# Kernel optimization log

Hardware: AMD Instinct MI355X
Metric: run time of the kernel (lower is better)

Reference implementation:

```python
import jax, jax.numpy as jnp
import numpy as np

N, K, M, H, F = 4, 1024, 1024, 16, 4096
D = M // H  # per-head dim (dim_q = dim_v = 64)
EPS = 1e-5


def _mha(q_in, k_in, v_in, Wq, bq, Wk, bk, Wv, bv, Wo, bo, mask):
    # Wq/Wk/Wv: [H, M, D]; bq/bk/bv: [H, D]; Wo: [H*D, M]; bo: [M]
    q = jnp.einsum('nkm,hmd->nhkd', q_in, Wq) + bq[None, :, None, :]
    k = jnp.einsum('nkm,hmd->nhkd', k_in, Wk) + bk[None, :, None, :]
    v = jnp.einsum('nkm,hmd->nhkd', v_in, Wv) + bv[None, :, None, :]
    scores = jnp.einsum('nhkd,nhld->nhkl', q, k) / jnp.sqrt(jnp.asarray(D, q.dtype))
    if mask is not None:
        scores = jnp.where(mask[:, None, :, :] == 0, jnp.asarray(-jnp.inf, q.dtype), scores)
    attn = jax.nn.softmax(scores, axis=-1)          # [N,H,K,K]
    y = jnp.einsum('nhkl,nhld->nhkd', attn, v)      # [N,H,K,D]
    y = y.transpose(0, 2, 1, 3).reshape(q_in.shape[0], q_in.shape[1], -1)  # concat heads -> [N,K,H*D]
    return y @ Wo + bo


def _ln(x, g, b):
    mu = jnp.mean(x, axis=-1, keepdims=True)
    var = jnp.mean((x - mu) ** 2, axis=-1, keepdims=True)
    return (x - mu) * jax.lax.rsqrt(var + EPS) * g + b


def setup_inputs() -> dict:
    key = jax.random.key(0)
    ks = jax.random.split(key, 24)
    s = 0.02
    def rn(k, shape):
        return jax.random.normal(k, shape, dtype=jnp.float32) * s
    inp = {
        'dec_inp': jax.random.normal(ks[0], (N, K, M), dtype=jnp.float32),
        'enc_out': jax.random.normal(ks[1], (N, K, M), dtype=jnp.float32),
        'mask': jnp.tril(jnp.ones((K, K), dtype=jnp.int32))[None].repeat(N, axis=0),
        # self-attention params
        'Wq_s': rn(ks[2], (H, M, D)), 'bq_s': jnp.zeros((H, D)),
        'Wk_s': rn(ks[3], (H, M, D)), 'bk_s': jnp.zeros((H, D)),
        'Wv_s': rn(ks[4], (H, M, D)), 'bv_s': jnp.zeros((H, D)),
        'Wo_s': rn(ks[5], (H * D, M)), 'bo_s': jnp.zeros((M,)),
        # cross-attention params
        'Wq_c': rn(ks[6], (H, M, D)), 'bq_c': jnp.zeros((H, D)),
        'Wk_c': rn(ks[7], (H, M, D)), 'bk_c': jnp.zeros((H, D)),
        'Wv_c': rn(ks[8], (H, M, D)), 'bv_c': jnp.zeros((H, D)),
        'Wo_c': rn(ks[9], (H * D, M)), 'bo_c': jnp.zeros((M,)),
        # feedforward params
        'W1': rn(ks[10], (M, F)), 'b1': jnp.zeros((F,)),
        'W2': rn(ks[11], (F, M)), 'b2': jnp.zeros((M,)),
        # layernorm params
        'g1': jnp.ones((M,)), 'be1': jnp.zeros((M,)),
        'g2': jnp.ones((M,)), 'be2': jnp.zeros((M,)),
        'g3': jnp.ones((M,)), 'be3': jnp.zeros((M,)),
    }
    return inp


def reference(dec_inp, enc_out, mask,
              Wq_s, bq_s, Wk_s, bk_s, Wv_s, bv_s, Wo_s, bo_s,
              Wq_c, bq_c, Wk_c, bk_c, Wv_c, bv_c, Wo_c, bo_c,
              W1, b1, W2, b2, g1, be1, g2, be2, g3, be3):
    # masked self-attention + residual + LN (dropout = identity in eval)
    out1 = _mha(dec_inp, dec_inp, dec_inp, Wq_s, bq_s, Wk_s, bk_s, Wv_s, bv_s, Wo_s, bo_s, mask)
    out2 = _ln(dec_inp + out1, g1, be1)
    # cross-attention with encoder output + residual + LN
    out3 = _mha(out2, enc_out, enc_out, Wq_c, bq_c, Wk_c, bk_c, Wv_c, bv_c, Wo_c, bo_c, None)
    out4 = _ln(out3 + out2, g2, be2)
    # feedforward + residual + LN
    out5 = jax.nn.relu(out4 @ W1 + b1) @ W2 + b2
    return _ln(out5 + out4, g3, be3)
```

## Files before the change

### kernel.cpp

```cpp
#include <hip/hip_runtime.h>

#define NB   4
#define SEQ  1024
#define MD   1024
#define NH   16
#define HD   64
#define FF   4096
#define NK   (NB*SEQ)
#define EPSF 1e-5f
#define QS   3072

typedef short short8 __attribute__((ext_vector_type(8)));
typedef float f32x4  __attribute__((ext_vector_type(4)));
typedef unsigned short u16;
typedef unsigned int u32;

__device__ __forceinline__ u16 f2bf(float x) {
    union { float f; unsigned u; } v; v.f = x;
    unsigned r = v.u + 0x7FFF + ((v.u >> 16) & 1);
    return (u16)(r >> 16);
}
__device__ __forceinline__ u16 f2bf_trunc(float x) {
    union { float f; unsigned u; } v; v.f = x;
    return (u16)(v.u >> 16);
}
__device__ __forceinline__ float bf2f(u16 x) {
    union { unsigned u; float f; } v; v.u = ((unsigned)x) << 16;
    return v.f;
}
__device__ __forceinline__ void gload_lds16(const void* g, void* l) {
    __builtin_amdgcn_global_load_lds(
        (const __attribute__((address_space(1))) unsigned int*)g,
        (__attribute__((address_space(3))) unsigned int*)l,
        16, 0, 0);
}

__global__ __launch_bounds__(256) void conv_bf16(const float* __restrict__ s0,
                                                 const float* __restrict__ s1,
                                                 u16* __restrict__ d0,
                                                 u16* __restrict__ d1) {
    const float* S = blockIdx.y ? s1 : s0;
    u16* D = blockIdx.y ? d1 : d0;
    const int i = blockIdx.x * 256 + threadIdx.x;
    float4 v = ((const float4*)S)[i];
    ushort4 o;
    o.x = f2bf(v.x); o.y = f2bf(v.y); o.z = f2bf(v.z); o.w = f2bf(v.w);
    ((ushort4*)D)[i] = o;
}

__global__ __launch_bounds__(256) void mask_tiles(const int* __restrict__ mask,
                                                  int* __restrict__ cls,
                                                  u32* __restrict__ bits) {
    const int jt = blockIdx.x, qt = blockIdx.y, n = blockIdx.z;
    const int t = threadIdx.x;
    const int r = t >> 1, h2 = (t & 1) * 2;
    u32 bb[2];
#pragma unroll
    for (int sg = 0; sg < 2; ++sg) {
        const int* mp = &mask[((size_t)n * SEQ + qt * 128 + r) * SEQ + jt * 128 + (h2 + sg) * 32];
        u32 b = 0;
#pragma unroll
        for (int k = 0; k < 8; ++k) {
            int4 v = *(const int4*)(mp + k * 4);
            b |= (v.x ? 1u : 0u) << (k * 4 + 0);
            b |= (v.y ? 1u : 0u) << (k * 4 + 1);
            b |= (v.z ? 1u : 0u) << (k * 4 + 2);
            b |= (v.w ? 1u : 0u) << (k * 4 + 3);
        }
        bb[sg] = b;
    }
    const int tile = (n * 8 + qt) * 8 + jt;
    bits[((size_t)tile * 128 + r) * 4 + h2]     = bb[0];
    bits[((size_t)tile * 128 + r) * 4 + h2 + 1] = bb[1];
    const int nfull  = __syncthreads_count(bb[0] == 0xFFFFFFFFu && bb[1] == 0xFFFFFFFFu);
    const int nempty = __syncthreads_count(bb[0] == 0u && bb[1] == 0u);
    if (t == 0) cls[tile] = (nfull == 256) ? 2 : ((nempty == 256) ? 0 : 1);
}

struct QkvArgs { const float* src[6]; u16* dst[6]; };

__global__ __launch_bounds__(256) void repack_qkv(QkvArgs a) {
    const int m0 = blockIdx.x * 64;
    const int h  = blockIdx.y;
    const int w  = blockIdx.z;
    const float* W = a.src[w];
    u16* BT = a.dst[w];
    const int t = threadIdx.x;
    __shared__ u16 Ts[64][72];

    const int r = t >> 4, c4 = (t & 15) * 4;
#pragma unroll
    for (int p = 0; p < 4; ++p) {
        const int row = r + p * 16;
        float4 v = *(const float4*)&W[((size_t)h * 1024 + m0 + row) * 64 + c4];
        Ts[row][c4] = f2bf(v.x); Ts[row][c4 + 1] = f2bf(v.y);
        Ts[row][c4 + 2] = f2bf(v.z); Ts[row][c4 + 3] = f2bf(v.w);
    }
    __syncthreads();
    const int d = t >> 2, j0 = (t & 3) * 16;
#pragma unroll
    for (int p = 0; p < 4; ++p) {
        ushort4 o;
        o.x = Ts[j0 + p * 4 + 0][d]; o.y = Ts[j0 + p * 4 + 1][d];
        o.z = Ts[j0 + p * 4 + 2][d]; o.w = Ts[j0 + p * 4 + 3][d];
        *(ushort4*)&BT[((size_t)h * 64 + d) * 1024 + m0 + j0 + p * 4] = o;
    }
}

struct FD { const float* src; int ss; u16* dst; int ds; };
struct FlatArgs { FD d[10]; };

__global__ __launch_bounds__(256) void repack_flat(FlatArgs fa) {
    FD u = fa.d[blockIdx.z];
    const int r0 = blockIdx.x * 64;
    const int c0 = blockIdx.y * 64;
    const int t  = threadIdx.x;
    __shared__ u16 Ts[64][72];

    const int r = t >> 4, c4 = (t & 15) * 4;
#pragma unroll
    for (int p = 0; p < 4; ++p) {
        const int row = r + p * 16;
        float4 v = *(const float4*)&u.src[(size_t)(r0 + row) * u.ss + c0 + c4];
        Ts[row][c4] = f2bf(v.x); Ts[row][c4 + 1] = f2bf(v.y);
        Ts[row][c4 + 2] = f2bf(v.z); Ts[row][c4 + 3] = f2bf(v.w);
    }
    __syncthreads();
    const int d = t >> 2, j0 = (t & 3) * 16;
#pragma unroll
    for (int p = 0; p < 4; ++p) {
        ushort4 o;
        o.x = Ts[j0 + p * 4 + 0][d]; o.y = Ts[j0 + p * 4 + 1][d];
        o.z = Ts[j0 + p * 4 + 2][d]; o.w = Ts[j0 + p * 4 + 3][d];
        *(ushort4*)&u.dst[(size_t)(c0 + d) * u.ds + r0 + j0 + p * 4] = o;
    }
}

template<int OUT_BF16, int RELU, int RESID, int BIAS3, int PARTIAL, int VT>
__global__ __launch_bounds__(256) void gemm_mfma(const u16* __restrict__ A,
                                                 const u16* __restrict__ A2,
                                                 int Astride,
                                                 const u16* __restrict__ BT,
                                                 int Bstride,
                                                 const float* __restrict__ b0,
                                                 const float* __restrict__ b1p,
                                                 const float* __restrict__ b2p,
                                                 const float* __restrict__ resid,
                                                 void* __restrict__ Cout,
                                                 u16* __restrict__ VtOut,
                                                 int Kd, int Nd) {
    const int nt = blockIdx.x;
    const int mt = blockIdx.y;
    const int t  = threadIdx.x;
    const int wave = t >> 6, lane = t & 63;
    const int q = lane >> 4, l16 = lane & 15;
    const int wm = wave >> 1, wn = wave & 1;

    __shared__ __align__(16) u16 As[128 * 64];
    __shared__ __align__(16) u16 Bs[128 * 64];

    const int row0 = mt * 128, col0 = nt * 128;
    const u16* Ause = (col0 < 1024) ? A : A2;
    const int kBase = PARTIAL ? blockIdx.z * Kd : 0;

    f32x4 acc[4][4];
#pragma unroll
    for (int r = 0; r < 4; ++r)
#pragma unroll
        for (int c = 0; c < 4; ++c) acc[r][c] = (f32x4)0.0f;

    const int lrow = lane >> 3;
    const int lcb  = lane & 7;

    for (int k0 = 0; k0 < Kd; k0 += 64) {
        __syncthreads();
#pragma unroll
        for (int p = 0; p < 4; ++p) {
            const int rr = wave * 32 + p * 8 + lrow;
            const int gcb = lcb ^ (rr & 7);
            gload_lds16(Ause + (size_t)(row0 + rr) * Astride + kBase + k0 + gcb * 8, As + (size_t)(wave * 32 + p * 8) * 64);
            gload_lds16(BT   + (size_t)(col0 + rr) * Bstride + kBase + k0 + gcb * 8, Bs + (size_t)(wave * 32 + p * 8) * 64);
        }
        __syncthreads();

#pragma unroll
        for (int s = 0; s < 2; ++s) {
            const int pb = (q + s * 4) ^ (l16 & 7);
            short8 af[4], bf[4];
#pragma unroll
            for (int r = 0; r < 4; ++r)
                af[r] = *(const short8*)&As[(wm * 64 + r * 16 + l16) * 64 + pb * 8];
#pragma unroll
            for (int c = 0; c < 4; ++c)
                bf[c] = *(const short8*)&Bs[(wn * 64 + c * 16 + l16) * 64 + pb * 8];
#pragma unroll
            for (int r = 0; r < 4; ++r)
#pragma unroll
                for (int c = 0; c < 4; ++c)
                    acc[r][c] = __builtin_amdgcn_mfma_f32_16x16x32_bf16(af[r], bf[c], acc[r][c], 0, 0, 0);
        }
    }

    float* Pout = PARTIAL ? ((float*)Cout + (size_t)blockIdx.z * NK * Nd) : nullptr;

#pragma unroll
    for (int c = 0; c < 4; ++c) {
        const int col = col0 + wn * 64 + c * 16 + l16;
        float bb = 0.0f;
        if (!PARTIAL) {
            if (BIAS3) {
                const int sec = col >> 10;
                const float* bp = sec == 0 ? b0 : (sec == 1 ? b1p : b2p);
                bb = bp[col & 1023];
            } else {
                bb = b0[col];
            }
        }
#pragma unroll
        for (int r = 0; r < 4; ++r) {
#pragma unroll
            for (int reg = 0; reg < 4; ++reg) {
                const int row = row0 + wm * 64 + r * 16 + q * 4 + reg;
                float v = acc[r][c][reg] + bb;
                if (PARTIAL) {
                    Pout[(size_t)row * Nd + col] = acc[r][c][reg];
                } else {
                    if (RELU)  v = fmaxf(v, 0.0f);
                    if (RESID) v += resid[(size_t)row * Nd + col];
                    if (OUT_BF16) ((u16*)Cout)[(size_t)row * Nd + col] = f2bf(v);
                    else          ((float*)Cout)[(size_t)row * Nd + col] = v;
                }
            }
        }
    }
}

template<int OUT_BF16, int RELU, int BIAS3, int PARTIAL, int VT>
__global__ __launch_bounds__(512, 2) void gemm256p(const u16* __restrict__ A,
                                                   const u16* __restrict__ A2,
                                                   int Astride,
                                                   const u16* __restrict__ BT,
                                                   int Bstride,
                                                   const float* __restrict__ b0,
                                                   const float* __restrict__ b1p,
                                                   const float* __restrict__ b2p,
                                                   void* __restrict__ Cout,
                                                   u16* __restrict__ VtOut,
                                                   int Kd, int Nd, int swzW) {
    const int t  = threadIdx.x;
    const int wave = t >> 6, lane = t & 63;
    const int q = lane >> 4, l16 = lane & 15;
    const int wm = wave >> 1, wn = wave & 1;
    const int x7 = l16 & 7;

    const int gx = gridDim.x;
    const int bid = blockIdx.x + blockIdx.y * gx;
    const int cpx = (gx * gridDim.y) >> 3;
    const int xcd = bid & 7;
    const int cc  = bid >> 3;
    const int regNX = gx / swzW;
    const int mtspan = cpx / swzW;
    const int nt = (xcd % regNX) * swzW + cc % swzW;
    const int mt = (xcd / regNX) * mtspan + cc / swzW;

    extern __shared__ __align__(16) char smem[];
    u16* As = (u16*)smem;
    u16* Bs = (u16*)(smem + 3 * 256 * 64 * 2);

    const int row0 = mt * 256, col0 = nt * 128;
    const u16* Ause = (col0 < 1024) ? A : A2;
    const int kBase = PARTIAL ? blockIdx.z * Kd : 0;

    f32x4 acc[4][4];
#pragma unroll
    for (int r = 0; r < 4; ++r)
#pragma unroll
        for (int c = 0; c < 4; ++c) acc[r][c] = (f32x4)0.0f;

    const int lrow = lane >> 3;
    const int lcb  = lane & 7;

    auto stagePart = [&](int slot, int kk, int part) {
#pragma unroll
        for (int p = 0; p < 2; ++p) {
            const int rr = wave * 32 + (part * 2 + p) * 8 + lrow;
            const int gcb = lcb ^ (rr & 7);
            gload_lds16(Ause + (size_t)(row0 + rr) * Astride + kk + gcb * 8,
                        As + slot * (256 * 64) + (wave * 32 + (part * 2 + p) * 8) * 64);
        }
        {
            const int rr = wave * 16 + part * 8 + lrow;
            const int gcb = lcb ^ (rr & 7);
            gload_lds16(BT + (size_t)(col0 + rr) * Bstride + kk + gcb * 8,
                        Bs + slot * (128 * 64) + (wave * 16 + part * 8) * 64);
        }
    };

    const int nsteps = Kd / 64;
    stagePart(0, kBase, 0);      stagePart(0, kBase, 1);
    stagePart(1, kBase + 64, 0); stagePart(1, kBase + 64, 1);

    int st = 0, st2 = 2;
    for (int it = 0; it < nsteps; ++it) {
        if (it + 1 < nsteps) asm volatile("s_waitcnt vmcnt(6)" ::: "memory");
        else                 asm volatile("s_waitcnt vmcnt(0)" ::: "memory");
        __builtin_amdgcn_s_barrier();

        const u16* Ab = As + st * (256 * 64);
        const u16* Bb = Bs + st * (128 * 64);
        const int pb0 = q ^ x7;
        const int pb1 = (q + 4) ^ x7;

        short8 af0[4], bf0[4], af1[4], bf1[4];
#pragma unroll
        for (int r = 0; r < 4; ++r) {
            af0[r] = *(const short8*)&Ab[(wm * 64 + r * 16 + l16) * 64 + pb0 * 8];
            af1[r] = *(const short8*)&Ab[(wm * 64 + r * 16 + l16) * 64 + pb1 * 8];
        }
#pragma unroll
        for (int c = 0; c < 4; ++c) {
            bf0[c] = *(const short8*)&Bb[(wn * 64 + c * 16 + l16) * 64 + pb0 * 8];
            bf1[c] = *(const short8*)&Bb[(wn * 64 + c * 16 + l16) * 64 + pb1 * 8];
        }

        const bool pre = (it + 2 < nsteps);
        const int kk2 = kBase + (it + 2) * 64;
        if (pre) stagePart(st2, kk2, 0);

        __builtin_amdgcn_s_setprio(1);
#pragma unroll
        for (int r = 0; r < 4; ++r)
#pragma unroll
            for (int c = 0; c < 4; ++c)
                acc[r][c] = __builtin_amdgcn_mfma_f32_16x16x32_bf16(af0[r], bf0[c], acc[r][c], 0, 0, 0);
        __builtin_amdgcn_s_setprio(0);

        if (pre) stagePart(st2, kk2, 1);

        __builtin_amdgcn_s_setprio(1);
#pragma unroll
        for (int r = 0; r < 4; ++r)
#pragma unroll
            for (int c = 0; c < 4; ++c)
                acc[r][c] = __builtin_amdgcn_mfma_f32_16x16x32_bf16(af1[r], bf1[c], acc[r][c], 0, 0, 0);
        __builtin_amdgcn_s_setprio(0);

        st  = (st  == 2) ? 0 : st + 1;
        st2 = (st2 == 2) ? 0 : st2 + 1;
    }

    if (VT && col0 >= 2048) {
#pragma unroll
        for (int c = 0; c < 4; ++c) {
            const int col = col0 + wn * 64 + c * 16 + l16;
            const float bb = b2p[col & 1023];
            const int d = col & 63, hh = (col >> 6) & 15;
#pragma unroll
            for (int r = 0; r < 4; ++r) {
                const int row = row0 + wm * 64 + r * 16 + q * 4;
                const int nn = row >> 10, k = row & 1023;
                ushort4 o;
                o.x = f2bf(acc[r][c][0] + bb);
                o.y = f2bf(acc[r][c][1] + bb);
                o.z = f2bf(acc[r][c][2] + bb);
                o.w = f2bf(acc[r][c][3] + bb);
                *(ushort4*)&VtOut[((size_t)(nn * 16 + hh) * 64 + d) * 1024 + k] = o;
            }
        }
        return;
    }

    float* Pout = PARTIAL ? ((float*)Cout + (size_t)blockIdx.z * NK * Nd) : nullptr;

#pragma unroll
    for (int c = 0; c < 4; ++c) {
        const int col = col0 + wn * 64 + c * 16 + l16;
        float bb = 0.0f;
        if (!PARTIAL) {
            if (BIAS3) {
                const int sec = col >> 10;
                const float* bp = sec == 0 ? b0 : (sec == 1 ? b1p : b2p);
                bb = bp[col & 1023];
            } else {
                bb = b0[col];
            }
        }
#pragma unroll
        for (int r = 0; r < 4; ++r) {
#pragma unroll
            for (int reg = 0; reg < 4; ++reg) {
                const int row = row0 + wm * 64 + r * 16 + q * 4 + reg;
                float v = acc[r][c][reg] + bb;
                if (PARTIAL) {
                    Pout[(size_t)row * Nd + col] = acc[r][c][reg];
                } else {
                    if (RELU)  v = fmaxf(v, 0.0f);
                    if (OUT_BF16) ((u16*)Cout)[(size_t)row * Nd + col] = f2bf(v);
                    else          ((float*)Cout)[(size_t)row * Nd + col] = v;
                }
            }
        }
    }
}

#define PSTR 136
#define ATTN_LDS (128*64*2 + 64*128*2 + 8*16*PSTR*2)

__global__ __launch_bounds__(512, 4) void attn_mfma(const u16* __restrict__ QKV,
                                                    const u16* __restrict__ Vt,
                                                    const int* __restrict__ cls,
                                                    const u32* __restrict__ bits,
                                                    u16* __restrict__ Yout) {
    const int h  = blockIdx.x;
    const int n  = blockIdx.z;
    const int qt = (n & 2) ? 7 - (int)blockIdx.y : (int)blockIdx.y;
    const int t  = threadIdx.x;
    const int wave = t >> 6;
    const int lane = t & 63;
    const int quad = lane >> 4;
    const int l16  = lane & 15;
    const int sw   = wave >> 2;
    const int wq   = wave & 3;

    extern __shared__ __align__(16) char smem[];
    u16* Ks = (u16*)smem;
    u16* Vs = (u16*)(smem + 128 * 64 * 2);
    u16* Pw = (u16*)(smem + 128 * 64 * 2 + 64 * 128 * 2) + wave * 16 * PSTR;

    const int bh = n * NH + h;
    const int i0 = qt * 128;

    int cl[8];
    if (cls) {
        const int* cp = &cls[(n * 8 + qt) * 8];
#pragma unroll
        for (int j = 0; j < 8; ++j) cl[j] = cp[j];
    } else {
#pragma unroll
        for (int j = 0; j < 8; ++j) cl[j] = 2;
    }

    short8 qf[2];
    {
        const u16* qrow = QKV + ((size_t)n * SEQ + i0 + sw * 64 + wq * 16 + l16) * QS + h * 64 + quad * 8;
        short8 a = *(const short8*)(qrow);
        short8 b = *(const short8*)(qrow + 32);
#pragma unroll
        for (int j = 0; j < 8; ++j) {
            qf[0][j] = (short)f2bf(bf2f((u16)a[j]) * 0.18033688f);
            qf[1][j] = (short)f2bf(bf2f((u16)b[j]) * 0.18033688f);
        }
    }

    f32x4 O[4];
#pragma unroll
    for (int d = 0; d < 4; ++d) O[d] = (f32x4)0.0f;
    float lrow[4] = {};

    const int krow = lane >> 3, kblk = lane & 7;
    const int vrow = lane >> 4, vblk = lane & 15;
    const int x7 = l16 & 7;

    for (int jt = 0; jt < SEQ / 128; ++jt) {
        const int c = cl[jt];
        if (c == 0) continue;
        __syncthreads();

#pragma unroll
        for (int p = 0; p < 2; ++p) {
            const int rr = wave * 16 + p * 8 + krow;
            const int kb = kblk ^ (rr & 7);
            gload_lds16(QKV + ((size_t)n * SEQ + jt * 128 + rr) * QS + 1024 + h * 64 + kb * 8,
                        Ks + (wave * 16 + p * 8) * 64);
        }
#pragma unroll
        for (int p = 0; p < 2; ++p) {
            const int rr = wave * 8 + p * 4 + vrow;
            const int kb = vblk ^ (rr & 15);
            gload_lds16(Vt + ((size_t)bh * HD + rr) * SEQ + jt * 128 + kb * 8,
                        Vs + (wave * 8 + p * 4) * 128);
        }
        __syncthreads();

        f32x4 S[8];
#pragma unroll
        for (int sub = 0; sub < 8; ++sub) {
            S[sub] = (f32x4)0.0f;
            const int row = sub * 16 + l16;
            short8 k0 = *(const short8*)&Ks[row * 64 + ((quad ^ x7) * 8)];
            S[sub] = __builtin_amdgcn_mfma_f32_16x16x32_bf16(qf[0], k0, S[sub], 0, 0, 0);
            short8 k1 = *(const short8*)&Ks[row * 64 + (((4 + quad) ^ x7) * 8)];
            S[sub] = __builtin_amdgcn_mfma_f32_16x16x32_bf16(qf[1], k1, S[sub], 0, 0, 0);
        }

        if (c == 1) {
#pragma unroll
            for (int reg = 0; reg < 4; ++reg) {
                const int row = sw * 64 + wq * 16 + quad * 4 + reg;
                const uint4 mm = *(const uint4*)&bits[((size_t)((n * 8 + qt) * 8 + jt) * 128 + row) * 4];
#pragma unroll
                for (int sub = 0; sub < 8; ++sub) {
                    const u32 seg = (sub >> 1) == 0 ? mm.x : (sub >> 1) == 1 ? mm.y : (sub >> 1) == 2 ? mm.z : mm.w;
                    if (!((seg >> ((sub & 1) * 16 + l16)) & 1u)) S[sub][reg] = -1e30f;
                }
            }
        }

#pragma unroll
        for (int reg = 0; reg < 4; ++reg) {
            float rs = 0.0f;
#pragma unroll
            for (int sub = 0; sub < 8; ++sub) {
                float e = exp2f(S[sub][reg]);
                Pw[(quad * 4 + reg) * PSTR + sub * 16 + l16] = f2bf_trunc(e);
                rs += e;
            }
            rs += __shfl_xor(rs, 1);
            rs += __shfl_xor(rs, 2);
            rs += __shfl_xor(rs, 4);
            rs += __shfl_xor(rs, 8);
            lrow[reg] += rs;
        }

        short8 pa[4];
#pragma unroll
        for (int ks = 0; ks < 4; ++ks)
            pa[ks] = *(const short8*)&Pw[l16 * PSTR + ks * 32 + quad * 8];
#pragma unroll
        for (int d = 0; d < 4; ++d) {
            const int row = d * 16 + l16;
#pragma unroll
            for (int ks = 0; ks < 4; ++ks) {
                short8 vb = *(const short8*)&Vs[row * 128 + (((ks * 4 + quad) ^ l16) & 15) * 8];
                O[d] = __builtin_amdgcn_mfma_f32_16x16x32_bf16(pa[ks], vb, O[d], 0, 0, 0);
            }
        }
    }

#pragma unroll
    for (int d = 0; d < 4; ++d) {
#pragma unroll
        for (int reg = 0; reg < 4; ++reg) {
            const int row = i0 + sw * 64 + wq * 16 + quad * 4 + reg;
            const int col = h * 64 + d * 16 + l16;
            Yout[((size_t)n * SEQ + row) * QS + col] = f2bf(O[d][reg] / lrow[reg]);
        }
    }
}

__global__ __launch_bounds__(256) void ln_kernel(const float* __restrict__ X,
                                                 const float* __restrict__ g,
                                                 const float* __restrict__ be,
                                                 float* __restrict__ Y,
                                                 u16* __restrict__ Yb) {
    const int row = blockIdx.x;
    const int t = threadIdx.x;
    __shared__ float red[256];

    const float4 v = ((const float4*)(X + (size_t)row * MD))[t];
    red[t] = v.x + v.y + v.z + v.w;
    __syncthreads();
    for (int s2 = 128; s2 > 0; s2 >>= 1) {
        if (t < s2) red[t] += red[t + s2];
        __syncthreads();
    }
    const float mu = red[0] * (1.0f / MD);
    __syncthreads();

    float dx = v.x - mu, dy = v.y - mu, dz = v.z - mu, dw = v.w - mu;
    red[t] = dx * dx + dy * dy + dz * dz + dw * dw;
    __syncthreads();
    for (int s2 = 128; s2 > 0; s2 >>= 1) {
        if (t < s2) red[t] += red[t + s2];
        __syncthreads();
    }
    const float var = red[0] * (1.0f / MD);
    const float rs = rsqrtf(var + EPSF);

    const float4 gv = ((const float4*)g)[t];
    const float4 bv = ((const float4*)be)[t];
    float4 o;
    o.x = dx * rs * gv.x + bv.x;
    o.y = dy * rs * gv.y + bv.y;
    o.z = dz * rs * gv.z + bv.z;
    o.w = dw * rs * gv.w + bv.w;
    if (Y) ((float4*)(Y + (size_t)row * MD))[t] = o;
    if (Yb) {
        ushort4 ob;
        ob.x = f2bf(o.x); ob.y = f2bf(o.y); ob.z = f2bf(o.z); ob.w = f2bf(o.w);
        ((ushort4*)(Yb + (size_t)row * MD))[t] = ob;
    }
}

__global__ __launch_bounds__(256) void ln_fused2(const float* __restrict__ p0,
                                                 const float* __restrict__ p1,
                                                 const float* __restrict__ bias,
                                                 const float* __restrict__ resid,
                                                 const float* __restrict__ g,
                                                 const float* __restrict__ be,
                                                 float* __restrict__ Y) {
    const int row = blockIdx.x;
    const int t = threadIdx.x;
    __shared__ float red[256];

    const float4 a = ((const float4*)(p0 + (size_t)row * MD))[t];
    const float4 b = ((const float4*)(p1 + (size_t)row * MD))[t];
    const float4 r = ((const float4*)(resid + (size_t)row * MD))[t];
    const float4 bi = ((const float4*)bias)[t];
    float4 v;
    v.x = a.x + b.x + r.x + bi.x;
    v.y = a.y + b.y + r.y + bi.y;
    v.z = a.z + b.z + r.z + bi.z;
    v.w = a.w + b.w + r.w + bi.w;

    red[t] = v.x + v.y + v.z + v.w;
    __syncthreads();
    for (int s2 = 128; s2 > 0; s2 >>= 1) {
        if (t < s2) red[t] += red[t + s2];
        __syncthreads();
    }
    const float mu = red[0] * (1.0f / MD);
    __syncthreads();

    float dx = v.x - mu, dy = v.y - mu, dz = v.z - mu, dw = v.w - mu;
    red[t] = dx * dx + dy * dy + dz * dz + dw * dw;
    __syncthreads();
    for (int s2 = 128; s2 > 0; s2 >>= 1) {
        if (t < s2) red[t] += red[t + s2];
        __syncthreads();
    }
    const float var = red[0] * (1.0f / MD);
    const float rs = rsqrtf(var + EPSF);

    const float4 gv = ((const float4*)g)[t];
    const float4 bv = ((const float4*)be)[t];
    float4 o;
    o.x = dx * rs * gv.x + bv.x;
    o.y = dy * rs * gv.y + bv.y;
    o.z = dz * rs * gv.z + bv.z;
    o.w = dw * rs * gv.w + bv.w;
    ((float4*)(Y + (size_t)row * MD))[t] = o;
}

extern "C" void kernel_launch(void* const* d_in, const int* in_sizes, int n_in,
                              void* d_out, int out_size, void* d_ws, size_t ws_size,
                              hipStream_t stream) {
    const float* dec  = (const float*)d_in[0];
    const float* enc  = (const float*)d_in[1];
    const int*   mask = (const int*)d_in[2];
    const float* Wq_s = (const float*)d_in[3];
    const float* bq_s = (const float*)d_in[4];
    const float* Wk_s = (const float*)d_in[5];
    const float* bk_s = (const float*)d_in[6];
    const float* Wv_s = (const float*)d_in[7];
    const float* bv_s = (const float*)d_in[8];
    const float* Wo_s = (const float*)d_in[9];
    const float* bo_s = (const float*)d_in[10];
    const float* Wq_c = (const float*)d_in[11];
    const float* bq_c = (const float*)d_in[12];
    const float* Wk_c = (const float*)d_in[13];
    const float* bk_c = (const float*)d_in[14];
    const float* Wv_c = (const float*)d_in[15];
    const float* bv_c = (const float*)d_in[16];
    const float* Wo_c = (const float*)d_in[17];
    const float* bo_c = (const float*)d_in[18];
    const float* W1   = (const float*)d_in[19];
    const float* b1   = (const float*)d_in[20];
    const float* W2   = (const float*)d_in[21];
    const float* b2   = (const float*)d_in[22];
    const float* g1   = (const float*)d_in[23];
    const float* be1  = (const float*)d_in[24];
    const float* g2   = (const float*)d_in[25];
    const float* be2  = (const float*)d_in[26];
    const float* g3   = (const float*)d_in[27];
    const float* be3  = (const float*)d_in[28];

    char* wsb = (char*)d_ws;
    const size_t MB = 1u << 20;
    u16*   decb  = (u16*)(wsb + 0 * MB);
    u16*   O2b   = (u16*)(wsb + 0 * MB);
    u16*   encb  = (u16*)(wsb + 8 * MB);
    u16*   O4b   = (u16*)(wsb + 8 * MB);
    u16*   WqkvsT= (u16*)(wsb + 16 * MB);
    u16*   WqkvcT= (u16*)(wsb + 22 * MB);
    u16*   WosT  = (u16*)(wsb + 28 * MB);
    u16*   WocT  = (u16*)(wsb + 30 * MB);
    u16*   W1T   = (u16*)(wsb + 32 * MB);
    u16*   W2T   = (u16*)(wsb + 40 * MB);
    u16*   QKVb  = (u16*)(wsb + 48 * MB);
    u16*   Vt    = (u16*)(wsb + 72 * MB);
    u16*   Hb    = (u16*)(wsb + 48 * MB);
    int*   mcls  = (int*)(wsb + 80 * MB);
    u32*   mbits = (u32*)(wsb + 80 * MB + 64 * 1024);
    float* Tb    = (float*)(wsb + 80 * MB);
    float* FP    = (float*)(wsb + 0 * MB);
    float* O2    = (float*)(wsb + 96 * MB);
    float* O4    = (float*)(wsb + 96 * MB);

    dim3 blk(256);
    dim3 blkA(512);
    dim3 blkG(512);
    dim3 gConv(NK * MD / 4 / 256, 2);
    dim3 gMask(8, 8, 4);
    dim3 gQkvW(16, 16, 6);
    dim3 gFlatW(16, 16, 10);
    dim3 gAttn(NH, SEQ / 128, NB);
    dim3 gQKV(QS / 128, NK / 256);
    dim3 gOut(MD / 128, NK / 128);
    dim3 gF1(FF / 128, NK / 256);
    dim3 gF2(MD / 128, NK / 256, 2);
    const int GP_LDS = 3 * (256 * 64 + 128 * 64) * 2;

    conv_bf16<<<gConv, blk, 0, stream>>>(dec, enc, decb, encb);
    mask_tiles<<<gMask, blk, 0, stream>>>(mask, mcls, mbits);

    QkvArgs qa;
    qa.src[0] = Wq_s; qa.src[1] = Wk_s; qa.src[2] = Wv_s;
    qa.src[3] = Wq_c; qa.src[4] = Wk_c; qa.src[5] = Wv_c;
    qa.dst[0] = WqkvsT;                 qa.dst[1] = WqkvsT + (size_t)1024 * 1024;
    qa.dst[2] = WqkvsT + (size_t)2048 * 1024;
    qa.dst[3] = WqkvcT;                 qa.dst[4] = WqkvcT + (size_t)1024 * 1024;
    qa.dst[5] = WqkvcT + (size_t)2048 * 1024;
    repack_qkv<<<gQkvW, blk, 0, stream>>>(qa);

    FlatArgs fa;
    fa.d[0] = { Wo_s, 1024, WosT, 1024 };
    fa.d[1] = { Wo_c, 1024, WocT, 1024 };
    for (int u = 0; u < 4; ++u)
        fa.d[2 + u] = { W1 + (size_t)u * 1024, 4096, W1T + (size_t)u * 1024 * 1024, 1024 };
    for (int u = 0; u < 4; ++u)
        fa.d[6 + u] = { W2 + (size_t)u * 1024 * 1024, 1024, W2T + (size_t)u * 1024, 4096 };
    repack_flat<<<gFlatW, blk, 0, stream>>>(fa);

    gemm256p<1, 0, 1, 0, 1><<<gQKV, blkG, GP_LDS, stream>>>(decb, decb, MD, WqkvsT, MD, bq_s, bk_s, bv_s, QKVb, Vt, MD, QS, 6);
    attn_mfma<<<gAttn, blkA, ATTN_LDS, stream>>>(QKVb, Vt, mcls, mbits, QKVb);
    gemm_mfma<0, 0, 1, 0, 0, 0><<<gOut, blk, 0, stream>>>(QKVb, QKVb, QS, WosT, MD, bo_s, nullptr, nullptr, dec, Tb, nullptr, MD, MD);
    ln_kernel<<<NK, blk, 0, stream>>>(Tb, g1, be1, O2, O2b);

    gemm256p<1, 0, 1, 0, 1><<<gQKV, blkG, GP_LDS, stream>>>(O2b, encb, MD, WqkvcT, MD, bq_c, bk_c, bv_c, QKVb, Vt, MD, QS, 6);
    attn_mfma<<<gAttn, blkA, ATTN_LDS, stream>>>(QKVb, Vt, nullptr, nullptr, QKVb);
    gemm_mfma<0, 0, 1, 0, 0, 0><<<gOut, blk, 0, stream>>>(QKVb, QKVb, QS, WocT, MD, bo_c, nullptr, nullptr, O2, Tb, nullptr, MD, MD);
    ln_kernel<<<NK, blk, 0, stream>>>(Tb, g2, be2, O4, O4b);

    gemm256p<1, 1, 0, 0, 0><<<gF1, blkG, GP_LDS, stream>>>(O4b, O4b, MD, W1T, MD, b1, nullptr, nullptr, Hb, nullptr, MD, FF, 8);
    gemm256p<0, 0, 0, 1, 0><<<gF2, blkG, GP_LDS, stream>>>(Hb, Hb, FF, W2T, FF, nullptr, nullptr, nullptr, FP, nullptr, FF / 2, MD, 2);
    ln_fused2<<<NK, blk, 0, stream>>>(FP, FP + (size_t)NK * MD, b2, O4, g3, be3, (float*)d_out);
}
```

Baseline: 325.0 us.

## Route output projections through pipelined GEMM and double-buffer attention K/V tiles

The output-projection GEMMs switch from the simple 128x128 kernel to the triple-buffered 256x128 kernel, which gains a residual-add template flag so the older kernel can be removed. The attention kernel now processes 64-wide key tiles with double-buffered async loads of K and V, prefetching the next tile while computing the current one. This targets load latency stalls in both kernels. The cost is more barriers per key tile in attention and fewer blocks in the output GEMMs (128 instead of 256), which may underfill the GPU.

```diff
diff --git a/kernel.cpp b/kernel.cpp
--- a/kernel.cpp
+++ b/kernel.cpp
@@ -136,30 +136,40 @@
     }
 }
 
-template<int OUT_BF16, int RELU, int RESID, int BIAS3, int PARTIAL, int VT>
-__global__ __launch_bounds__(256) void gemm_mfma(const u16* __restrict__ A,
-                                                 const u16* __restrict__ A2,
-                                                 int Astride,
-                                                 const u16* __restrict__ BT,
-                                                 int Bstride,
-                                                 const float* __restrict__ b0,
-                                                 const float* __restrict__ b1p,
-                                                 const float* __restrict__ b2p,
-                                                 const float* __restrict__ resid,
-                                                 void* __restrict__ Cout,
-                                                 u16* __restrict__ VtOut,
-                                                 int Kd, int Nd) {
-    const int nt = blockIdx.x;
-    const int mt = blockIdx.y;
+template<int OUT_BF16, int RELU, int BIAS3, int PARTIAL, int VT, int RESID>
+__global__ __launch_bounds__(512, 2) void gemm256p(const u16* __restrict__ A,
+                                                   const u16* __restrict__ A2,
+                                                   int Astride,
+                                                   const u16* __restrict__ BT,
+                                                   int Bstride,
+                                                   const float* __restrict__ b0,
+                                                   const float* __restrict__ b1p,
+                                                   const float* __restrict__ b2p,
+                                                   const float* __restrict__ resid,
+                                                   void* __restrict__ Cout,
+                                                   u16* __restrict__ VtOut,
+                                                   int Kd, int Nd, int swzW) {
     const int t  = threadIdx.x;
     const int wave = t >> 6, lane = t & 63;
     const int q = lane >> 4, l16 = lane & 15;
     const int wm = wave >> 1, wn = wave & 1;
-
-    __shared__ __align__(16) u16 As[128 * 64];
-    __shared__ __align__(16) u16 Bs[128 * 64];
-
-    const int row0 = mt * 128, col0 = nt * 128;
+    const int x7 = l16 & 7;
+
+    const int gx = gridDim.x;
+    const int bid = blockIdx.x + blockIdx.y * gx;
+    const int cpx = (gx * gridDim.y) >> 3;
+    const int xcd = bid & 7;
+    const int cc  = bid >> 3;
+    const int regNX = gx / swzW;
+    const int mtspan = cpx / swzW;
+    const int nt = (xcd % regNX) * swzW + cc % swzW;
+    const int mt = (xcd / regNX) * mtspan + cc / swzW;
+
+    extern __shared__ __align__(16) char smem[];
+    u16* As = (u16*)smem;
+    u16* Bs = (u16*)(smem + 3 * 256 * 64 * 2);
+
+    const int row0 = mt * 256, col0 = nt * 128;
     const u16* Ause = (col0 < 1024) ? A : A2;
     const int kBase = PARTIAL ? blockIdx.z * Kd : 0;
 
@@ -172,33 +182,94 @@
     const int lrow = lane >> 3;
     const int lcb  = lane & 7;
 
-    for (int k0 = 0; k0 < Kd; k0 += 64) {
-        __syncthreads();
-#pragma unroll
-        for (int p = 0; p < 4; ++p) {
-            const int rr = wave * 32 + p * 8 + lrow;
+    auto stagePart = [&](int slot, int kk, int part) {
+#pragma unroll
+        for (int p = 0; p < 2; ++p) {
+            const int rr = wave * 32 + (part * 2 + p) * 8 + lrow;
             const int gcb = lcb ^ (rr & 7);
-            gload_lds16(Ause + (size_t)(row0 + rr) * Astride + kBase + k0 + gcb * 8, As + (size_t)(wave * 32 + p * 8) * 64);
-            gload_lds16(BT   + (size_t)(col0 + rr) * Bstride + kBase + k0 + gcb * 8, Bs + (size_t)(wave * 32 + p * 8) * 64);
-        }
-        __syncthreads();
-
-#pragma unroll
-        for (int s = 0; s < 2; ++s) {
-            const int pb = (q + s * 4) ^ (l16 & 7);
-            short8 af[4], bf[4];
-#pragma unroll
-            for (int r = 0; r < 4; ++r)
-                af[r] = *(const short8*)&As[(wm * 64 + r * 16 + l16) * 64 + pb * 8];
+            gload_lds16(Ause + (size_t)(row0 + rr) * Astride + kk + gcb * 8,
+                        As + slot * (256 * 64) + (wave * 32 + (part * 2 + p) * 8) * 64);
+        }
+        {
+            const int rr = wave * 16 + part * 8 + lrow;
+            const int gcb = lcb ^ (rr & 7);
+            gload_lds16(BT + (size_t)(col0 + rr) * Bstride + kk + gcb * 8,
+                        Bs + slot * (128 * 64) + (wave * 16 + part * 8) * 64);
+        }
+    };
+
+    const int nsteps = Kd / 64;
+    stagePart(0, kBase, 0);      stagePart(0, kBase, 1);
+    stagePart(1, kBase + 64, 0); stagePart(1, kBase + 64, 1);
+
+    int st = 0, st2 = 2;
+    for (int it = 0; it < nsteps; ++it) {
+        if (it + 1 < nsteps) asm volatile("s_waitcnt vmcnt(6)" ::: "memory");
+        else                 asm volatile("s_waitcnt vmcnt(0)" ::: "memory");
+        __builtin_amdgcn_s_barrier();
+
+        const u16* Ab = As + st * (256 * 64);
+        const u16* Bb = Bs + st * (128 * 64);
+        const int pb0 = q ^ x7;
+        const int pb1 = (q + 4) ^ x7;
+
+        short8 af0[4], bf0[4], af1[4], bf1[4];
+#pragma unroll
+        for (int r = 0; r < 4; ++r) {
+            af0[r] = *(const short8*)&Ab[(wm * 64 + r * 16 + l16) * 64 + pb0 * 8];
+            af1[r] = *(const short8*)&Ab[(wm * 64 + r * 16 + l16) * 64 + pb1 * 8];
+        }
+#pragma unroll
+        for (int c = 0; c < 4; ++c) {
+            bf0[c] = *(const short8*)&Bb[(wn * 64 + c * 16 + l16) * 64 + pb0 * 8];
+            bf1[c] = *(const short8*)&Bb[(wn * 64 + c * 16 + l16) * 64 + pb1 * 8];
+        }
+
+        const bool pre = (it + 2 < nsteps);
+        const int kk2 = kBase + (it + 2) * 64;
+        if (pre) stagePart(st2, kk2, 0);
+
+        __builtin_amdgcn_s_setprio(1);
+#pragma unroll
+        for (int r = 0; r < 4; ++r)
 #pragma unroll
             for (int c = 0; c < 4; ++c)
-                bf[c] = *(const short8*)&Bs[(wn * 64 + c * 16 + l16) * 64 + pb * 8];
-#pragma unroll
-            for (int r = 0; r < 4; ++r)
-#pragma unroll
-                for (int c = 0; c < 4; ++c)
-                    acc[r][c] = __builtin_amdgcn_mfma_f32_16x16x32_bf16(af[r], bf[c], acc[r][c], 0, 0, 0);
-        }
+                acc[r][c] = __builtin_amdgcn_mfma_f32_16x16x32_bf16(af0[r], bf0[c], acc[r][c], 0, 0, 0);
+        __builtin_amdgcn_s_setprio(0);
+
+        if (pre) stagePart(st2, kk2, 1);
+
+        __builtin_amdgcn_s_setprio(1);
+#pragma unroll
+        for (int r = 0; r < 4; ++r)
+#pragma unroll
+            for (int c = 0; c < 4; ++c)
+                acc[r][c] = __builtin_amdgcn_mfma_f32_16x16x32_bf16(af1[r], bf1[c], acc[r][c], 0, 0, 0);
+        __builtin_amdgcn_s_setprio(0);
+
+        st  = (st  == 2) ? 0 : st + 1;
+        st2 = (st2 == 2) ? 0 : st2 + 1;
+    }
+
+    if (VT && col0 >= 2048) {
+#pragma unroll
+        for (int c = 0; c < 4; ++c) {
+            const int col = col0 + wn * 64 + c * 16 + l16;
+            const float bb = b2p[col & 1023];
+            const int d = col & 63, hh = (col >> 6) & 15;
+#pragma unroll
+            for (int r = 0; r < 4; ++r) {
+                const int row = row0 + wm * 64 + r * 16 + q * 4;
+                const int nn = row >> 10, k = row & 1023;
+                ushort4 o;
+                o.x = f2bf(acc[r][c][0] + bb);
+                o.y = f2bf(acc[r][c][1] + bb);
+                o.z = f2bf(acc[r][c][2] + bb);
+                o.w = f2bf(acc[r][c][3] + bb);
+                *(ushort4*)&VtOut[((size_t)(nn * 16 + hh) * 64 + d) * 1024 + k] = o;
+            }
+        }
+        return;
     }
 
     float* Pout = PARTIAL ? ((float*)Cout + (size_t)blockIdx.z * NK * Nd) : nullptr;
@@ -235,176 +306,8 @@
     }
 }
 
-template<int OUT_BF16, int RELU, int BIAS3, int PARTIAL, int VT>
-__global__ __launch_bounds__(512, 2) void gemm256p(const u16* __restrict__ A,
-                                                   const u16* __restrict__ A2,
-                                                   int Astride,
-                                                   const u16* __restrict__ BT,
-                                                   int Bstride,
-                                                   const float* __restrict__ b0,
-                                                   const float* __restrict__ b1p,
-                                                   const float* __restrict__ b2p,
-                                                   void* __restrict__ Cout,
-                                                   u16* __restrict__ VtOut,
-                                                   int Kd, int Nd, int swzW) {
-    const int t  = threadIdx.x;
-    const int wave = t >> 6, lane = t & 63;
-    const int q = lane >> 4, l16 = lane & 15;
-    const int wm = wave >> 1, wn = wave & 1;
-    const int x7 = l16 & 7;
-
-    const int gx = gridDim.x;
-    const int bid = blockIdx.x + blockIdx.y * gx;
-    const int cpx = (gx * gridDim.y) >> 3;
-    const int xcd = bid & 7;
-    const int cc  = bid >> 3;
-    const int regNX = gx / swzW;
-    const int mtspan = cpx / swzW;
-    const int nt = (xcd % regNX) * swzW + cc % swzW;
-    const int mt = (xcd / regNX) * mtspan + cc / swzW;
-
-    extern __shared__ __align__(16) char smem[];
-    u16* As = (u16*)smem;
-    u16* Bs = (u16*)(smem + 3 * 256 * 64 * 2);
-
-    const int row0 = mt * 256, col0 = nt * 128;
-    const u16* Ause = (col0 < 1024) ? A : A2;
-    const int kBase = PARTIAL ? blockIdx.z * Kd : 0;
-
-    f32x4 acc[4][4];
-#pragma unroll
-    for (int r = 0; r < 4; ++r)
-#pragma unroll
-        for (int c = 0; c < 4; ++c) acc[r][c] = (f32x4)0.0f;
-
-    const int lrow = lane >> 3;
-    const int lcb  = lane & 7;
-
-    auto stagePart = [&](int slot, int kk, int part) {
-#pragma unroll
-        for (int p = 0; p < 2; ++p) {
-            const int rr = wave * 32 + (part * 2 + p) * 8 + lrow;
-            const int gcb = lcb ^ (rr & 7);
-            gload_lds16(Ause + (size_t)(row0 + rr) * Astride + kk + gcb * 8,
-                        As + slot * (256 * 64) + (wave * 32 + (part * 2 + p) * 8) * 64);
-        }
-        {
-            const int rr = wave * 16 + part * 8 + lrow;
-            const int gcb = lcb ^ (rr & 7);
-            gload_lds16(BT + (size_t)(col0 + rr) * Bstride + kk + gcb * 8,
-                        Bs + slot * (128 * 64) + (wave * 16 + part * 8) * 64);
-        }
-    };
-
-    const int nsteps = Kd / 64;
-    stagePart(0, kBase, 0);      stagePart(0, kBase, 1);
-    stagePart(1, kBase + 64, 0); stagePart(1, kBase + 64, 1);
-
-    int st = 0, st2 = 2;
-    for (int it = 0; it < nsteps; ++it) {
-        if (it + 1 < nsteps) asm volatile("s_waitcnt vmcnt(6)" ::: "memory");
-        else                 asm volatile("s_waitcnt vmcnt(0)" ::: "memory");
-        __builtin_amdgcn_s_barrier();
-
-        const u16* Ab = As + st * (256 * 64);
-        const u16* Bb = Bs + st * (128 * 64);
-        const int pb0 = q ^ x7;
-        const int pb1 = (q + 4) ^ x7;
-
-        short8 af0[4], bf0[4], af1[4], bf1[4];
-#pragma unroll
-        for (int r = 0; r < 4; ++r) {
-            af0[r] = *(const short8*)&Ab[(wm * 64 + r * 16 + l16) * 64 + pb0 * 8];
-            af1[r] = *(const short8*)&Ab[(wm * 64 + r * 16 + l16) * 64 + pb1 * 8];
-        }
-#pragma unroll
-        for (int c = 0; c < 4; ++c) {
-            bf0[c] = *(const short8*)&Bb[(wn * 64 + c * 16 + l16) * 64 + pb0 * 8];
-            bf1[c] = *(const short8*)&Bb[(wn * 64 + c * 16 + l16) * 64 + pb1 * 8];
-        }
-
-        const bool pre = (it + 2 < nsteps);
-        const int kk2 = kBase + (it + 2) * 64;
-        if (pre) stagePart(st2, kk2, 0);
-
-        __builtin_amdgcn_s_setprio(1);
-#pragma unroll
-        for (int r = 0; r < 4; ++r)
-#pragma unroll
-            for (int c = 0; c < 4; ++c)
-                acc[r][c] = __builtin_amdgcn_mfma_f32_16x16x32_bf16(af0[r], bf0[c], acc[r][c], 0, 0, 0);
-        __builtin_amdgcn_s_setprio(0);
-
-        if (pre) stagePart(st2, kk2, 1);
-
-        __builtin_amdgcn_s_setprio(1);
-#pragma unroll
-        for (int r = 0; r < 4; ++r)
-#pragma unroll
-            for (int c = 0; c < 4; ++c)
-                acc[r][c] = __builtin_amdgcn_mfma_f32_16x16x32_bf16(af1[r], bf1[c], acc[r][c], 0, 0, 0);
-        __builtin_amdgcn_s_setprio(0);
-
-        st  = (st  == 2) ? 0 : st + 1;
-        st2 = (st2 == 2) ? 0 : st2 + 1;
-    }
-
-    if (VT && col0 >= 2048) {
-#pragma unroll
-        for (int c = 0; c < 4; ++c) {
-            const int col = col0 + wn * 64 + c * 16 + l16;
-            const float bb = b2p[col & 1023];
-            const int d = col & 63, hh = (col >> 6) & 15;
-#pragma unroll
-            for (int r = 0; r < 4; ++r) {
-                const int row = row0 + wm * 64 + r * 16 + q * 4;
-                const int nn = row >> 10, k = row & 1023;
-                ushort4 o;
-                o.x = f2bf(acc[r][c][0] + bb);
-                o.y = f2bf(acc[r][c][1] + bb);
-                o.z = f2bf(acc[r][c][2] + bb);
-                o.w = f2bf(acc[r][c][3] + bb);
-                *(ushort4*)&VtOut[((size_t)(nn * 16 + hh) * 64 + d) * 1024 + k] = o;
-            }
-        }
-        return;
-    }
-
-    float* Pout = PARTIAL ? ((float*)Cout + (size_t)blockIdx.z * NK * Nd) : nullptr;
-
-#pragma unroll
-    for (int c = 0; c < 4; ++c) {
-        const int col = col0 + wn * 64 + c * 16 + l16;
-        float bb = 0.0f;
-        if (!PARTIAL) {
-            if (BIAS3) {
-                const int sec = col >> 10;
-                const float* bp = sec == 0 ? b0 : (sec == 1 ? b1p : b2p);
-                bb = bp[col & 1023];
-            } else {
-                bb = b0[col];
-            }
-        }
-#pragma unroll
-        for (int r = 0; r < 4; ++r) {
-#pragma unroll
-            for (int reg = 0; reg < 4; ++reg) {
-                const int row = row0 + wm * 64 + r * 16 + q * 4 + reg;
-                float v = acc[r][c][reg] + bb;
-                if (PARTIAL) {
-                    Pout[(size_t)row * Nd + col] = acc[r][c][reg];
-                } else {
-                    if (RELU)  v = fmaxf(v, 0.0f);
-                    if (OUT_BF16) ((u16*)Cout)[(size_t)row * Nd + col] = f2bf(v);
-                    else          ((float*)Cout)[(size_t)row * Nd + col] = v;
-                }
-            }
-        }
-    }
-}
-
-#define PSTR 136
-#define ATTN_LDS (128*64*2 + 64*128*2 + 8*16*PSTR*2)
+#define PSTR 72
+#define ATTN_LDS (2*64*64*2 + 2*64*64*2 + 8*16*PSTR*2)
 
 __global__ __launch_bounds__(512, 4) void attn_mfma(const u16* __restrict__ QKV,
                                                     const u16* __restrict__ Vt,
@@ -421,11 +324,12 @@
     const int l16  = lane & 15;
     const int sw   = wave >> 2;
     const int wq   = wave & 3;
+    const int x7   = l16 & 7;
 
     extern __shared__ __align__(16) char smem[];
     u16* Ks = (u16*)smem;
-    u16* Vs = (u16*)(smem + 128 * 64 * 2);
-    u16* Pw = (u16*)(smem + 128 * 64 * 2 + 64 * 128 * 2) + wave * 16 * PSTR;
+    u16* Vs = (u16*)(smem + 2 * 64 * 64 * 2);
+    u16* Pw = (u16*)(smem + 4 * 64 * 64 * 2) + wave * 16 * PSTR;
 
     const int bh = n * NH + h;
     const int i0 = qt * 128;
@@ -439,6 +343,9 @@
 #pragma unroll
         for (int j = 0; j < 8; ++j) cl[j] = 2;
     }
+    int na = 0;
+#pragma unroll
+    for (int j = 0; j < 8; ++j) if (cl[j] != 0) na += 2;
 
     short8 qf[2];
     {
@@ -457,50 +364,52 @@
     for (int d = 0; d < 4; ++d) O[d] = (f32x4)0.0f;
     float lrow[4] = {};
 
-    const int krow = lane >> 3, kblk = lane & 7;
-    const int vrow = lane >> 4, vblk = lane & 15;
-    const int x7 = l16 & 7;
-
-    for (int jt = 0; jt < SEQ / 128; ++jt) {
-        const int c = cl[jt];
-        if (c == 0) continue;
-        __syncthreads();
-
-#pragma unroll
-        for (int p = 0; p < 2; ++p) {
-            const int rr = wave * 16 + p * 8 + krow;
-            const int kb = kblk ^ (rr & 7);
-            gload_lds16(QKV + ((size_t)n * SEQ + jt * 128 + rr) * QS + 1024 + h * 64 + kb * 8,
-                        Ks + (wave * 16 + p * 8) * 64);
-        }
-#pragma unroll
-        for (int p = 0; p < 2; ++p) {
-            const int rr = wave * 8 + p * 4 + vrow;
-            const int kb = vblk ^ (rr & 15);
-            gload_lds16(Vt + ((size_t)bh * HD + rr) * SEQ + jt * 128 + kb * 8,
-                        Vs + (wave * 8 + p * 4) * 128);
-        }
-        __syncthreads();
-
-        f32x4 S[8];
-#pragma unroll
-        for (int sub = 0; sub < 8; ++sub) {
+    const int srow = t >> 3;
+    const int scb  = t & 7;
+    const int skb  = scb ^ (srow & 7);
+
+    auto stageT = [&](int j, int b) {
+        gload_lds16(QKV + ((size_t)n * SEQ + j * 64 + srow) * QS + 1024 + h * 64 + skb * 8,
+                    Ks + b * 4096 + wave * 512);
+        gload_lds16(Vt + ((size_t)bh * HD + srow) * SEQ + j * 64 + skb * 8,
+                    Vs + b * 4096 + wave * 512);
+    };
+
+    stageT(0, 0);
+    int b = 0;
+    for (int i = 0; i < na; ++i) {
+        const int j = i;
+        const int cc = cl[j >> 1];
+        if (i + 1 < na) {
+            stageT(i + 1, b ^ 1);
+            asm volatile("s_waitcnt vmcnt(2)" ::: "memory");
+        } else {
+            asm volatile("s_waitcnt vmcnt(0)" ::: "memory");
+        }
+        __builtin_amdgcn_s_barrier();
+
+        const u16* Kb = Ks + b * 4096;
+        const u16* Vb = Vs + b * 4096;
+
+        f32x4 S[4];
+#pragma unroll
+        for (int sub = 0; sub < 4; ++sub) {
             S[sub] = (f32x4)0.0f;
             const int row = sub * 16 + l16;
-            short8 k0 = *(const short8*)&Ks[row * 64 + ((quad ^ x7) * 8)];
+            short8 k0 = *(const short8*)&Kb[row * 64 + ((quad ^ x7) * 8)];
             S[sub] = __builtin_amdgcn_mfma_f32_16x16x32_bf16(qf[0], k0, S[sub], 0, 0, 0);
-            short8 k1 = *(const short8*)&Ks[row * 64 + (((4 + quad) ^ x7) * 8)];
+            short8 k1 = *(const short8*)&Kb[row * 64 + (((4 + quad) ^ x7) * 8)];
             S[sub] = __builtin_amdgcn_mfma_f32_16x16x32_bf16(qf[1], k1, S[sub], 0, 0, 0);
         }
 
-        if (c == 1) {
+        if (cc == 1) {
 #pragma unroll
             for (int reg = 0; reg < 4; ++reg) {
                 const int row = sw * 64 + wq * 16 + quad * 4 + reg;
-                const uint4 mm = *(const uint4*)&bits[((size_t)((n * 8 + qt) * 8 + jt) * 128 + row) * 4];
-#pragma unroll
-                for (int sub = 0; sub < 8; ++sub) {
-                    const u32 seg = (sub >> 1) == 0 ? mm.x : (sub >> 1) == 1 ? mm.y : (sub >> 1) == 2 ? mm.z : mm.w;
+                const uint2 mm = *(const uint2*)&bits[((size_t)((n * 8 + qt) * 8 + (j >> 1)) * 128 + row) * 4 + (j & 1) * 2];
+#pragma unroll
+                for (int sub = 0; sub < 4; ++sub) {
+                    const u32 seg = (sub & 2) ? mm.y : mm.x;
                     if (!((seg >> ((sub & 1) * 16 + l16)) & 1u)) S[sub][reg] = -1e30f;
                 }
             }
@@ -510,7 +419,7 @@
         for (int reg = 0; reg < 4; ++reg) {
             float rs = 0.0f;
 #pragma unroll
-            for (int sub = 0; sub < 8; ++sub) {
+            for (int sub = 0; sub < 4; ++sub) {
                 float e = exp2f(S[sub][reg]);
                 Pw[(quad * 4 + reg) * PSTR + sub * 16 + l16] = f2bf_trunc(e);
                 rs += e;
@@ -522,19 +431,21 @@
             lrow[reg] += rs;
         }
 
-        short8 pa[4];
-#pragma unroll
-        for (int ks = 0; ks < 4; ++ks)
+        short8 pa[2];
+#pragma unroll
+        for (int ks = 0; ks < 2; ++ks)
             pa[ks] = *(const short8*)&Pw[l16 * PSTR + ks * 32 + quad * 8];
 #pragma unroll
         for (int d = 0; d < 4; ++d) {
             const int row = d * 16 + l16;
 #pragma unroll
-            for (int ks = 0; ks < 4; ++ks) {
-                short8 vb = *(const short8*)&Vs[row * 128 + (((ks * 4 + quad) ^ l16) & 15) * 8];
+            for (int ks = 0; ks < 2; ++ks) {
+                short8 vb = *(const short8*)&Vb[row * 64 + (((ks * 4 + quad) ^ x7) & 7) * 8];
                 O[d] = __builtin_amdgcn_mfma_f32_16x16x32_bf16(pa[ks], vb, O[d], 0, 0, 0);
             }
         }
+        __builtin_amdgcn_s_barrier();
+        b ^= 1;
     }
 
 #pragma unroll
@@ -706,7 +617,7 @@
     dim3 gFlatW(16, 16, 10);
     dim3 gAttn(NH, SEQ / 128, NB);
     dim3 gQKV(QS / 128, NK / 256);
-    dim3 gOut(MD / 128, NK / 128);
+    dim3 gOut256(MD / 128, NK / 256);
     dim3 gF1(FF / 128, NK / 256);
     dim3 gF2(MD / 128, NK / 256, 2);
     const int GP_LDS = 3 * (256 * 64 + 128 * 64) * 2;
@@ -732,17 +643,17 @@
         fa.d[6 + u] = { W2 + (size_t)u * 1024 * 1024, 1024, W2T + (size_t)u * 1024, 4096 };
     repack_flat<<<gFlatW, blk, 0, stream>>>(fa);
 
-    gemm256p<1, 0, 1, 0, 1><<<gQKV, blkG, GP_LDS, stream>>>(decb, decb, MD, WqkvsT, MD, bq_s, bk_s, bv_s, QKVb, Vt, MD, QS, 6);
+    gemm256p<1, 0, 1, 0, 1, 0><<<gQKV, blkG, GP_LDS, stream>>>(decb, decb, MD, WqkvsT, MD, bq_s, bk_s, bv_s, nullptr, QKVb, Vt, MD, QS, 6);
     attn_mfma<<<gAttn, blkA, ATTN_LDS, stream>>>(QKVb, Vt, mcls, mbits, QKVb);
-    gemm_mfma<0, 0, 1, 0, 0, 0><<<gOut, blk, 0, stream>>>(QKVb, QKVb, QS, WosT, MD, bo_s, nullptr, nullptr, dec, Tb, nullptr, MD, MD);
+    gemm256p<0, 0, 0, 0, 0, 1><<<gOut256, blkG, GP_LDS, stream>>>(QKVb, QKVb, QS, WosT, MD, bo_s, nullptr, nullptr, dec, Tb, nullptr, MD, MD, 2);
     ln_kernel<<<NK, blk, 0, stream>>>(Tb, g1, be1, O2, O2b);
 
-    gemm256p<1, 0, 1, 0, 1><<<gQKV, blkG, GP_LDS, stream>>>(O2b, encb, MD, WqkvcT, MD, bq_c, bk_c, bv_c, QKVb, Vt, MD, QS, 6);
+    gemm256p<1, 0, 1, 0, 1, 0><<<gQKV, blkG, GP_LDS, stream>>>(O2b, encb, MD, WqkvcT, MD, bq_c, bk_c, bv_c, nullptr, QKVb, Vt, MD, QS, 6);
     attn_mfma<<<gAttn, blkA, ATTN_LDS, stream>>>(QKVb, Vt, nullptr, nullptr, QKVb);
-    gemm_mfma<0, 0, 1, 0, 0, 0><<<gOut, blk, 0, stream>>>(QKVb, QKVb, QS, WocT, MD, bo_c, nullptr, nullptr, O2, Tb, nullptr, MD, MD);
+    gemm256p<0, 0, 0, 0, 0, 1><<<gOut256, blkG, GP_LDS, stream>>>(QKVb, QKVb, QS, WocT, MD, bo_c, nullptr, nullptr, O2, Tb, nullptr, MD, MD, 2);
     ln_kernel<<<NK, blk, 0, stream>>>(Tb, g2, be2, O4, O4b);
 
-    gemm256p<1, 1, 0, 0, 0><<<gF1, blkG, GP_LDS, stream>>>(O4b, O4b, MD, W1T, MD, b1, nullptr, nullptr, Hb, nullptr, MD, FF, 8);
-    gemm256p<0, 0, 0, 1, 0><<<gF2, blkG, GP_LDS, stream>>>(Hb, Hb, FF, W2T, FF, nullptr, nullptr, nullptr, FP, nullptr, FF / 2, MD, 2);
+    gemm256p<1, 1, 0, 0, 0, 0><<<gF1, blkG, GP_LDS, stream>>>(O4b, O4b, MD, W1T, MD, b1, nullptr, nullptr, nullptr, Hb, nullptr, MD, FF, 8);
+    gemm256p<0, 0, 0, 1, 0, 0><<<gF2, blkG, GP_LDS, stream>>>(Hb, Hb, FF, W2T, FF, nullptr, nullptr, nullptr, nullptr, FP, nullptr, FF / 2, MD, 2);
     ln_fused2<<<NK, blk, 0, stream>>>(FP, FP + (size_t)NK * MD, b2, O4, g3, be3, (float*)d_out);
 }
```

After: 328.2 us. Within noise of the previous version (+1.0%).
